# Kernel optimization log

Measured on AMD Instinct MI355X. Metric: run time of the kernel, lower is better.

## Reference

```python
import jax, jax.numpy as jnp
import numpy as np


def _conv3x3(x, w):
    # x: [B,Cin,H,W], w: [Cout,Cin,3,3], stride 1, pad 1
    return jax.lax.conv_general_dilated(x, w, window_strides=(1, 1), padding='SAME',
                                        dimension_numbers=('NCHW', 'OIHW', 'NCHW'))


def _affine(x, s, b):
    # per-channel folded eval-mode BatchNorm (+ absorbed conv bias)
    return x * s[None, :, None, None] + b[None, :, None, None]


def _lif_encode(h, thr, beta, T=4):
    # LIF integrate-and-fire scan: membrane = beta*m + h; STE spike; soft reset.
    def step(m, _):
        m = beta * m + h
        sig = jax.nn.sigmoid(4.0 * (m - thr))
        hard = (m > thr).astype(h.dtype)
        spk = sig + jax.lax.stop_gradient(hard - sig)  # surrogate-gradient STE
        return m - spk * thr, spk
    _, spikes = jax.lax.scan(step, jnp.zeros_like(h), None, length=T)
    return spikes  # [T,B,C_bot,H,W]


def _level(feat, ew, ebs, ebb, thr, braw, dw, dbs, dbb):
    h = _affine(_conv3x3(feat, ew), ebs, ebb)
    spikes = _lif_encode(h, thr, jax.nn.sigmoid(braw))
    avg = spikes.mean(axis=0)  # ber=0.0 -> BSC channel is identity
    return jax.nn.silu(_affine(_conv3x3(avg, dw), dbs, dbb))


def _forward(feat3, enc3_w, enc3_bn_s, enc3_bn_b, enc3_thr, enc3_beta_raw, dec3_w, dec3_bn_s, dec3_bn_b,
             feat4, enc4_w, enc4_bn_s, enc4_bn_b, enc4_thr, enc4_beta_raw, dec4_w, dec4_bn_s, dec4_bn_b,
             feat5, enc5_w, enc5_bn_s, enc5_bn_b, enc5_thr, enc5_beta_raw, dec5_w, dec5_bn_s, dec5_bn_b):
    r3 = _level(feat3, enc3_w, enc3_bn_s, enc3_bn_b, enc3_thr, enc3_beta_raw, dec3_w, dec3_bn_s, dec3_bn_b)
    r4 = _level(feat4, enc4_w, enc4_bn_s, enc4_bn_b, enc4_thr, enc4_beta_raw, dec4_w, dec4_bn_s, dec4_bn_b)
    r5 = _level(feat5, enc5_w, enc5_bn_s, enc5_bn_b, enc5_thr, enc5_beta_raw, dec5_w, dec5_bn_s, dec5_bn_b)
    return (r3, r4, r5)


def setup_inputs() -> dict:
    key = jax.random.key(0)
    C_bot, B = 36, 16
    levels = {3: (64, 160), 4: (128, 80), 5: (256, 40)}
    inp = {}
    k = key
    for lvl, (c, s) in levels.items():
        k, k1, k2, k3 = jax.random.split(k, 4)
        inp[f'feat{lvl}'] = jax.random.normal(k1, (B, c, s, s), jnp.float32)
        inp[f'enc{lvl}_w'] = jax.random.normal(k2, (C_bot, c, 3, 3), jnp.float32) / np.float32(np.sqrt(9 * c))
        inp[f'enc{lvl}_bn_s'] = jnp.ones((C_bot,), jnp.float32)
        inp[f'enc{lvl}_bn_b'] = jnp.zeros((C_bot,), jnp.float32)
        inp[f'enc{lvl}_thr'] = jnp.ones((1, C_bot, 1, 1), jnp.float32)
        inp[f'enc{lvl}_beta_raw'] = jnp.full((1, C_bot, 1, 1), 2.2, jnp.float32)
        inp[f'dec{lvl}_w'] = jax.random.normal(k3, (c, C_bot, 3, 3), jnp.float32) / np.float32(np.sqrt(9 * C_bot))
        inp[f'dec{lvl}_bn_s'] = jnp.ones((c,), jnp.float32)
        inp[f'dec{lvl}_bn_b'] = jnp.zeros((c,), jnp.float32)
    return inp


def reference(feat3, enc3_w, enc3_bn_s, enc3_bn_b, enc3_thr, enc3_beta_raw, dec3_w, dec3_bn_s, dec3_bn_b,
              feat4, enc4_w, enc4_bn_s, enc4_bn_b, enc4_thr, enc4_beta_raw, dec4_w, dec4_bn_s, dec4_bn_b,
              feat5, enc5_w, enc5_bn_s, enc5_bn_b, enc5_thr, enc5_beta_raw, dec5_w, dec5_bn_s, dec5_bn_b):
    return _forward(feat3, enc3_w, enc3_bn_s, enc3_bn_b, enc3_thr, enc3_beta_raw, dec3_w, dec3_bn_s, dec3_bn_b,
                    feat4, enc4_w, enc4_bn_s, enc4_bn_b, enc4_thr, enc4_beta_raw, dec4_w, dec4_bn_s, dec4_bn_b,
                    feat5, enc5_w, enc5_bn_s, enc5_bn_b, enc5_thr, enc5_beta_raw, dec5_w, dec5_bn_s, dec5_bn_b)
```

## Files before the change

### kernel.cpp

```cpp
#include <hip/hip_runtime.h>
#include <hip/hip_bf16.h>

typedef __attribute__((ext_vector_type(8)))  short short8v;
typedef __attribute__((ext_vector_type(16))) float f32x16;
typedef __attribute__((ext_vector_type(4)))  int   int4v;

template<int CIN>
__global__ __launch_bounds__(256) void pack_we(
    const float* __restrict__ w, __hip_bfloat16* __restrict__ whi,
    __hip_bfloat16* __restrict__ wlo, int total)
{
    const int NCHUNK = CIN / 16;
    int idx = blockIdx.x * 256 + threadIdx.x;
    if (idx >= total) return;
    int m  = idx & 31;
    int h  = (idx >> 5) & 1;
    int s  = (idx >> 6) % 9;
    int c  = (idx / 576) % NCHUNK;
    int cg = idx / (576 * NCHUNK);
    int co = cg * 32 + m;
    unsigned short vh[8], vl[8];
    #pragma unroll
    for (int j = 0; j < 8; ++j) {
        int ci = c * 16 + h * 8 + j;
        float x = (co < 36) ? w[(long)co * CIN * 9 + ci * 9 + s] : 0.f;
        __hip_bfloat16 xh = __float2bfloat16(x);
        float rem = x - __bfloat162float(xh);
        __hip_bfloat16 xl = __float2bfloat16(rem);
        vh[j] = *(unsigned short*)&xh;
        vl[j] = *(unsigned short*)&xl;
    }
    *(int4v*)(whi + (long)idx * 8) = *(int4v*)vh;
    *(int4v*)(wlo + (long)idx * 8) = *(int4v*)vl;
}

template<int CIN>
__global__ __launch_bounds__(256) void feat_cl(
    const float* __restrict__ f, __hip_bfloat16* __restrict__ fh,
    __hip_bfloat16* __restrict__ fl, int HW, int npx)
{
    __shared__ float t[CIN][64];
    const int p0 = blockIdx.x * 64;

    for (int i = threadIdx.x; i < CIN * 64; i += 256) {
        int ci = i >> 6, px = i & 63;
        int p = p0 + px;
        float v = 0.f;
        if (p < npx) {
            int b = p / HW, r = p - b * HW;
            v = f[((long)b * CIN + ci) * HW + r];
        }
        t[ci][px] = v;
    }
    __syncthreads();

    for (int i = threadIdx.x; i < 64 * (CIN / 8); i += 256) {
        int px = i & 63, oct = i >> 6;
        int p = p0 + px;
        if (p >= npx) continue;
        unsigned short vh[8], vl[8];
        #pragma unroll
        for (int j = 0; j < 8; ++j) {
            float v = t[oct * 8 + j][px];
            __hip_bfloat16 xh = __float2bfloat16(v);
            float rem = v - __bfloat162float(xh);
            __hip_bfloat16 xl = __float2bfloat16(rem);
            vh[j] = *(unsigned short*)&xh;
            vl[j] = *(unsigned short*)&xl;
        }
        *(int4v*)(fh + (long)p * CIN + oct * 8) = *(int4v*)vh;
        *(int4v*)(fl + (long)p * CIN + oct * 8) = *(int4v*)vl;
    }
}

template<int CIN>
__global__ __launch_bounds__(256) void enc_mfma_cl(
    const __hip_bfloat16* __restrict__ fh,
    const __hip_bfloat16* __restrict__ fl,
    const __hip_bfloat16* __restrict__ whi,
    const __hip_bfloat16* __restrict__ wlo,
    const float* __restrict__ bn_s, const float* __restrict__ bn_b,
    const float* __restrict__ thr, const float* __restrict__ beta_raw,
    __hip_bfloat16* __restrict__ avg,
    int H, int W, int tiles_x)
{
    const int NCHUNK = CIN / 16;
    __shared__ __align__(16) short sbuf[324 * 48];
    short* hi_t = sbuf;
    short* lo_t = sbuf + 324 * 24;

    const int tid = threadIdx.x;
    const int b   = blockIdx.y;
    const int tx0 = (blockIdx.x % tiles_x) * 16;
    const int ty0 = (blockIdx.x / tiles_x) * 16;

    const int lane = tid & 63;
    const int wv   = tid >> 6;
    const int h    = lane >> 5;
    const int n    = lane & 31;
    const int lx   = n & 15;
    const int ly0  = wv * 4 + (n >> 4);

    f32x16 acc[2][2];
    #pragma unroll
    for (int cg = 0; cg < 2; ++cg)
        #pragma unroll
        for (int pf = 0; pf < 2; ++pf)
            #pragma unroll
            for (int k = 0; k < 16; ++k) acc[cg][pf][k] = 0.f;

    const char* aph = (const char*)whi + h * 512 + n * 16;
    const char* apl = (const char*)wlo + h * 512 + n * 16;
    const long  cgstride = (long)NCHUNK * 9216;

    for (int c = 0; c < NCHUNK; ++c) {
        for (int i = tid; i < 648; i += 256) {
            int p   = i >> 1, oct = i & 1;
            int hy = p / 18, hx = p - hy * 18;
            int gy = ty0 + hy - 1, gx = tx0 + hx - 1;
            int4v vh = {0, 0, 0, 0}, vl = {0, 0, 0, 0};
            if (gy >= 0 && gy < H && gx >= 0 && gx < W) {
                long pp = ((long)(b * H + gy) * W + gx) * CIN + c * 16 + oct * 8;
                vh = *(const int4v*)(fh + pp);
                vl = *(const int4v*)(fl + pp);
            }
            *(int4v*)((char*)hi_t + p * 48 + oct * 16) = vh;
            *(int4v*)((char*)lo_t + p * 48 + oct * 16) = vl;
        }
        __syncthreads();

        const char* ahc = aph + (long)c * 9216;
        const char* alc = apl + (long)c * 9216;
        #pragma unroll
        for (int s = 0; s < 9; ++s) {
            const int dy = s / 3, dx = s % 3;
            const int p0 = (ly0 + dy) * 18 + (lx + dx);
            const int p1 = p0 + 36;
            short8v bh0 = *(const short8v*)((const char*)hi_t + p0 * 48 + h * 16);
            short8v bh1 = *(const short8v*)((const char*)hi_t + p1 * 48 + h * 16);
            short8v bl0 = *(const short8v*)((const char*)lo_t + p0 * 48 + h * 16);
            short8v bl1 = *(const short8v*)((const char*)lo_t + p1 * 48 + h * 16);
            #pragma unroll
            for (int cg = 0; cg < 2; ++cg) {
                short8v af = *(const short8v*)(ahc + cg * cgstride + s * 1024);
                short8v al = *(const short8v*)(alc + cg * cgstride + s * 1024);
                acc[cg][0] = __builtin_amdgcn_mfma_f32_32x32x16_bf16(af, bh0, acc[cg][0], 0, 0, 0);
                acc[cg][0] = __builtin_amdgcn_mfma_f32_32x32x16_bf16(af, bl0, acc[cg][0], 0, 0, 0);
                acc[cg][0] = __builtin_amdgcn_mfma_f32_32x32x16_bf16(al, bh0, acc[cg][0], 0, 0, 0);
                acc[cg][1] = __builtin_amdgcn_mfma_f32_32x32x16_bf16(af, bh1, acc[cg][1], 0, 0, 0);
                acc[cg][1] = __builtin_amdgcn_mfma_f32_32x32x16_bf16(af, bl1, acc[cg][1], 0, 0, 0);
                acc[cg][1] = __builtin_amdgcn_mfma_f32_32x32x16_bf16(al, bh1, acc[cg][1], 0, 0, 0);
            }
        }
        __syncthreads();
    }

    for (int i = tid; i < 1280; i += 256)
        *(int4v*)((char*)sbuf + i * 16) = (int4v){0, 0, 0, 0};
    __syncthreads();

    #pragma unroll
    for (int cg = 0; cg < 2; ++cg) {
        #pragma unroll
        for (int r = 0; r < 16; ++r) {
            const int co = (cg << 5) + (r & 3) + ((r >> 2) << 3) + (h << 2);
            if (co < 36) {
                const float sc   = bn_s[co], sb = bn_b[co];
                const float beta = 1.f / (1.f + expf(-beta_raw[co]));
                const float t    = thr[co];
                #pragma unroll
                for (int pf = 0; pf < 2; ++pf) {
                    const int ly = ly0 + pf * 2;
                    float hv = acc[cg][pf][r] * sc + sb;
                    float m = 0.f, c2 = 0.f;
                    #pragma unroll
                    for (int s4 = 0; s4 < 4; ++s4) {
                        m = beta * m + hv;
                        if (m > t) { c2 += 1.f; m -= t; }
                    }
                    __hip_bfloat16 ov = __float2bfloat16(c2 * 0.25f);
                    sbuf[(ly * 16 + lx) * 40 + co] = *(short*)&ov;
                }
            }
        }
    }
    __syncthreads();

    const long tilebase = ((long)(b * H + ty0) * W + tx0) * 40;
    for (int i = tid; i < 1280; i += 256) {
        int px = i / 5, u = i - px * 5;
        int py2 = px >> 4, px2 = px & 15;
        *(int4v*)(avg + tilebase + ((long)py2 * W + px2) * 40 + u * 8) =
            *(const int4v*)(sbuf + px * 40 + u * 8);
    }
}

template<int CIN>
__global__ __launch_bounds__(256) void enc_mfma(
    const float* __restrict__ feat,
    const __hip_bfloat16* __restrict__ whi,
    const __hip_bfloat16* __restrict__ wlo,
    const float* __restrict__ bn_s, const float* __restrict__ bn_b,
    const float* __restrict__ thr, const float* __restrict__ beta_raw,
    __hip_bfloat16* __restrict__ avg,
    int H, int W, int tiles_x)
{
    const int NCHUNK = CIN / 16;
    __shared__ __align__(16) short hi_t[324 * 24];
    __shared__ __align__(16) short lo_t[324 * 24];

    const int tid = threadIdx.x;
    const int b   = blockIdx.y;
    const int tx0 = (blockIdx.x % tiles_x) * 16;
    const int ty0 = (blockIdx.x / tiles_x) * 16;

    const int lane = tid & 63;
    const int wv   = tid >> 6;
    const int h    = lane >> 5;
    const int n    = lane & 31;
    const int lx   = n & 15;
    const int ly0  = wv * 4 + (n >> 4);

    f32x16 acc[2][2];
    #pragma unroll
    for (int cg = 0; cg < 2; ++cg)
        #pragma unroll
        for (int pf = 0; pf < 2; ++pf)
            #pragma unroll
            for (int k = 0; k < 16; ++k) acc[cg][pf][k] = 0.f;

    const float* fb = feat + (long)b * CIN * H * W;
    const char* aph = (const char*)whi + h * 512 + n * 16;
    const char* apl = (const char*)wlo + h * 512 + n * 16;
    const long  cgstride = (long)NCHUNK * 9216;

    for (int c = 0; c < NCHUNK; ++c) {
        for (int i = tid; i < 324 * 16; i += 256) {
            int cil = i / 324;
            int p   = i - cil * 324;
            int hy = p / 18, hx = p - hy * 18;
            int gy = ty0 + hy - 1, gx = tx0 + hx - 1;
            float v = 0.f;
            if (gy >= 0 && gy < H && gx >= 0 && gx < W)
                v = fb[((long)(c * 16 + cil) * H + gy) * W + gx];
            __hip_bfloat16 vh = __float2bfloat16(v);
            float rem = v - __bfloat162float(vh);
            __hip_bfloat16 vl = __float2bfloat16(rem);
            hi_t[p * 24 + cil] = *(short*)&vh;
            lo_t[p * 24 + cil] = *(short*)&vl;
        }
        __syncthreads();

        const char* ahc = aph + (long)c * 9216;
        const char* alc = apl + (long)c * 9216;
        #pragma unroll
        for (int s = 0; s < 9; ++s) {
            const int dy = s / 3, dx = s % 3;
            const int p0 = (ly0 + dy) * 18 + (lx + dx);
            const int p1 = p0 + 36;
            short8v bh0 = *(const short8v*)((const char*)hi_t + p0 * 48 + h * 16);
            short8v bh1 = *(const short8v*)((const char*)hi_t + p1 * 48 + h * 16);
            short8v bl0 = *(const short8v*)((const char*)lo_t + p0 * 48 + h * 16);
            short8v bl1 = *(const short8v*)((const char*)lo_t + p1 * 48 + h * 16);
            #pragma unroll
            for (int cg = 0; cg < 2; ++cg) {
                short8v af = *(const short8v*)(ahc + cg * cgstride + s * 1024);
                short8v al = *(const short8v*)(alc + cg * cgstride + s * 1024);
                acc[cg][0] = __builtin_amdgcn_mfma_f32_32x32x16_bf16(af, bh0, acc[cg][0], 0, 0, 0);
                acc[cg][0] = __builtin_amdgcn_mfma_f32_32x32x16_bf16(af, bl0, acc[cg][0], 0, 0, 0);
                acc[cg][0] = __builtin_amdgcn_mfma_f32_32x32x16_bf16(al, bh0, acc[cg][0], 0, 0, 0);
                acc[cg][1] = __builtin_amdgcn_mfma_f32_32x32x16_bf16(af, bh1, acc[cg][1], 0, 0, 0);
                acc[cg][1] = __builtin_amdgcn_mfma_f32_32x32x16_bf16(af, bl1, acc[cg][1], 0, 0, 0);
                acc[cg][1] = __builtin_amdgcn_mfma_f32_32x32x16_bf16(al, bh1, acc[cg][1], 0, 0, 0);
            }
        }
        __syncthreads();
    }

    #pragma unroll
    for (int cg = 0; cg < 2; ++cg) {
        #pragma unroll
        for (int r = 0; r < 16; ++r) {
            const int co = (cg << 5) + (r & 3) + ((r >> 2) << 3) + (h << 2);
            if (co < 36) {
                const float sc   = bn_s[co], sb = bn_b[co];
                const float beta = 1.f / (1.f + expf(-beta_raw[co]));
                const float t    = thr[co];
                #pragma unroll
                for (int pf = 0; pf < 2; ++pf) {
                    const int gy = ty0 + ly0 + pf * 2, gx = tx0 + lx;
                    float hv = acc[cg][pf][r] * sc + sb;
                    float m = 0.f, c2 = 0.f;
                    #pragma unroll
                    for (int s4 = 0; s4 < 4; ++s4) {
                        m = beta * m + hv;
                        if (m > t) { c2 += 1.f; m -= t; }
                    }
                    if (gy < H && gx < W)
                        avg[((long)(b * H + gy) * W + gx) * 40 + co] =
                            __float2bfloat16(c2 * 0.25f);
                }
            }
        }
    }
}

template<int CIN, int CIPER, int CICHUNK, int COCHUNK, int TDIM, bool PARTIAL, bool CL>
__global__ __launch_bounds__(TDIM* TDIM) void enc_tiled(
    const float* __restrict__ feat,
    const float* __restrict__ w,
    const float* __restrict__ bn_s, const float* __restrict__ bn_b,
    const float* __restrict__ thr, const float* __restrict__ beta_raw,
    __hip_bfloat16* __restrict__ avg,
    float* __restrict__ partial,
    int H, int W, int tiles_x)
{
    const int TPB  = TDIM * TDIM;
    const int HALOD = TDIM + 2;
    const int NCO  = 36 / COCHUNK;
    __shared__ float fs[CICHUNK][HALOD][HALOD];

    const int tile = blockIdx.x;
    const int b    = blockIdx.y;
    const int coc  = blockIdx.z % NCO;
    const int cis  = blockIdx.z / NCO;
    const int co0  = coc * COCHUNK;
    const int tx0  = (tile % tiles_x) * TDIM;
    const int ty0  = (tile / tiles_x) * TDIM;

    const int tx = threadIdx.x % TDIM;
    const int ty = threadIdx.x / TDIM;
    const int ox = tx0 + tx, oy = ty0 + ty;

    float acc[COCHUNK];
    #pragma unroll
    for (int c = 0; c < COCHUNK; ++c) acc[c] = 0.f;

    const float* fb = feat + (long)b * CIN * H * W;
    const int ci_base = cis * CIPER;

    for (int cc = ci_base; cc < ci_base + CIPER; cc += CICHUNK) {
        for (int i = threadIdx.x; i < CICHUNK * HALOD * HALOD; i += TPB) {
            int ci = i / (HALOD * HALOD);
            int r  = i % (HALOD * HALOD);
            int hy = r / HALOD, hx = r % HALOD;
            int gy = ty0 + hy - 1, gx = tx0 + hx - 1;
            float v = 0.f;
            if (gy >= 0 && gy < H && gx >= 0 && gx < W)
                v = fb[((long)(cc + ci) * H + gy) * W + gx];
            fs[ci][hy][hx] = v;
        }
        __syncthreads();

        for (int ci = 0; ci < CICHUNK; ++ci) {
            float f0 = fs[ci][ty    ][tx], f1 = fs[ci][ty    ][tx+1], f2 = fs[ci][ty    ][tx+2];
            float f3 = fs[ci][ty + 1][tx], f4 = fs[ci][ty + 1][tx+1], f5 = fs[ci][ty + 1][tx+2];
            float f6 = fs[ci][ty + 2][tx], f7 = fs[ci][ty + 2][tx+1], f8 = fs[ci][ty + 2][tx+2];
            const float* wq = w + (long)(cc + ci) * 9;
            #pragma unroll
            for (int j = 0; j < COCHUNK; ++j) {
                const float* ww = wq + (long)(co0 + j) * CIN * 9;
                acc[j] += f0 * ww[0] + f1 * ww[1] + f2 * ww[2]
                        + f3 * ww[3] + f4 * ww[4] + f5 * ww[5]
                        + f6 * ww[6] + f7 * ww[7] + f8 * ww[8];
            }
        }
        __syncthreads();
    }

    if (ox < W && oy < H) {
        if (PARTIAL) {
            #pragma unroll
            for (int j = 0; j < COCHUNK; ++j)
                partial[((((long)cis * 16 + b) * 36 + (co0 + j)) * H + oy) * W + ox] = acc[j];
        } else {
            float cnt[COCHUNK];
            #pragma unroll
            for (int j = 0; j < COCHUNK; ++j) {
                int co = co0 + j;
                float hh   = acc[j] * bn_s[co] + bn_b[co];
                float beta = 1.f / (1.f + expf(-beta_raw[co]));
                float t    = thr[co];
                float m = 0.f, c2 = 0.f;
                #pragma unroll
                for (int s = 0; s < 4; ++s) {
                    m = beta * m + hh;
                    if (m > t) { c2 += 1.f; m -= t; }
                }
                cnt[j] = c2 * 0.25f;
            }
            if (CL) {
                unsigned* dp = (unsigned*)(avg + ((long)(b * H + oy) * W + ox) * 40 + co0);
                #pragma unroll
                for (int j2 = 0; j2 < COCHUNK / 2; ++j2) {
                    __hip_bfloat16 h0 = __float2bfloat16(cnt[2 * j2]);
                    __hip_bfloat16 h1 = __float2bfloat16(cnt[2 * j2 + 1]);
                    unsigned u0 = *(unsigned short*)&h0;
                    unsigned u1 = *(unsigned short*)&h1;
                    dp[j2] = u0 | (u1 << 16);
                }
            } else {
                #pragma unroll
                for (int j = 0; j < COCHUNK; ++j)
                    avg[(((long)b * 36 + (co0 + j)) * H + oy) * W + ox] = __float2bfloat16(cnt[j]);
            }
        }
    }
}

template<int SPLITS, bool CL>
__global__ __launch_bounds__(256) void combine_lif(
    const float* __restrict__ partial,
    const float* __restrict__ bn_s, const float* __restrict__ bn_b,
    const float* __restrict__ thr, const float* __restrict__ beta_raw,
    __hip_bfloat16* __restrict__ avg, int H, int W, int total)
{
    int idx = blockIdx.x * 256 + threadIdx.x;
    if (idx >= total) return;
    int HW = H * W;
    int co = (idx / HW) % 36;
    float hh = 0.f;
    #pragma unroll
    for (int s = 0; s < SPLITS; ++s) hh += partial[(long)s * total + idx];
    hh = hh * bn_s[co] + bn_b[co];
    float beta = 1.f / (1.f + expf(-beta_raw[co]));
    float t    = thr[co];
    float m = 0.f, cnt = 0.f;
    #pragma unroll
    for (int s = 0; s < 4; ++s) {
        m = beta * m + hh;
        if (m > t) { cnt += 1.f; m -= t; }
    }
    if (CL) {
        int b = idx / (36 * HW);
        int rem = idx % HW;
        int y = rem / W, x = rem % W;
        avg[((long)(b * H + y) * W + x) * 40 + co] = __float2bfloat16(cnt * 0.25f);
    } else {
        avg[idx] = __float2bfloat16(cnt * 0.25f);
    }
}

__global__ __launch_bounds__(256) void pack_w(
    const float* __restrict__ w, __hip_bfloat16* __restrict__ ap, int total)
{
    int idx = blockIdx.x * 256 + threadIdx.x;
    if (idx >= total) return;
    int m  = idx & 31;
    int h  = (idx >> 5) & 1;
    int s  = (idx >> 6) % 23;
    int cg = idx / (23 * 64);
    int o  = 2 * s + h;
    int co = cg * 32 + m;
    unsigned short v[8];
    #pragma unroll
    for (int j = 0; j < 8; ++j) {
        float x = 0.f;
        if (o < 45) {
            int tap = o / 5, oct = o % 5, ci = oct * 8 + j;
            if (ci < 36) x = w[(long)co * 324 + ci * 9 + tap];
        }
        __hip_bfloat16 hv = __float2bfloat16(x);
        v[j] = *(unsigned short*)&hv;
    }
    *(int4v*)(ap + (long)idx * 8) = *(int4v*)v;
}

template<int COG>
__global__ __launch_bounds__(256) void dec_mfma(
    const __hip_bfloat16* __restrict__ avg_cl,
    const __hip_bfloat16* __restrict__ apack,
    const float* __restrict__ bn_s, const float* __restrict__ bn_b,
    float* __restrict__ out, int Cout, int H, int W, int tiles_x)
{
    __shared__ __hip_bfloat16 tile[12960];

    const int tid    = threadIdx.x;
    const int b      = blockIdx.y;
    const int cgbase = blockIdx.z * COG;
    const int tx0 = (blockIdx.x % tiles_x) * 16;
    const int ty0 = (blockIdx.x / tiles_x) * 16;

    {
        const __hip_bfloat16* ab = avg_cl + (long)b * H * W * 40;
        for (int i = tid; i < 1620; i += 256) {
            int row = i / 90, u = i - row * 90;
            int px = u / 5, un = u - px * 5;
            int gy = ty0 + row - 1, gx = tx0 + px - 1;
            int4v v = {0, 0, 0, 0};
            if (gy >= 0 && gy < H && gx >= 0 && gx < W)
                v = *(const int4v*)(ab + ((long)gy * W + gx) * 40 + un * 8);
            *(int4v*)(tile + (row * 18 + px) * 40 + un * 8) = v;
        }
    }
    __syncthreads();

    const int lane = tid & 63;
    const int wv   = tid >> 6;
    const int h    = lane >> 5;
    const int n    = lane & 31;
    const int lx   = n & 15;
    const int ly0  = wv * 4 + (n >> 4);

    const char* tb  = (const char*)tile;
    const int   bb0 = ((ly0 + 1) * 18 + (lx + 1)) * 80;
    const int   bb1 = bb0 + 2 * 18 * 80;

    const char* ap = (const char*)apack + (long)cgbase * 23552 + h * 512 + n * 16;

    f32x16 acc[COG][2];
    #pragma unroll
    for (int cg = 0; cg < COG; ++cg)
        #pragma unroll
        for (int pf = 0; pf < 2; ++pf)
            #pragma unroll
            for (int k = 0; k < 16; ++k) acc[cg][pf][k] = 0.f;

    #pragma unroll
    for (int s = 0; s < 23; ++s) {
        int o0 = 2 * s;     if (o0 > 44) o0 = 44;
        int o1 = 2 * s + 1; if (o1 > 44) o1 = 44;
        const int C0 = ((o0 / 5) / 3 - 1) * 1440 + ((o0 / 5) % 3 - 1) * 80 + (o0 % 5) * 16;
        const int C1 = ((o1 / 5) / 3 - 1) * 1440 + ((o1 / 5) % 3 - 1) * 80 + (o1 % 5) * 16;
        const int offc = h ? C1 : C0;
        short8v bf0 = *(const short8v*)(tb + (bb0 + offc));
        short8v bf1 = *(const short8v*)(tb + (bb1 + offc));
        #pragma unroll
        for (int cg = 0; cg < COG; ++cg) {
            short8v af = *(const short8v*)(ap + cg * 23552 + s * 1024);
            acc[cg][0] = __builtin_amdgcn_mfma_f32_32x32x16_bf16(af, bf0, acc[cg][0], 0, 0, 0);
            acc[cg][1] = __builtin_amdgcn_mfma_f32_32x32x16_bf16(af, bf1, acc[cg][1], 0, 0, 0);
        }
    }

    #pragma unroll
    for (int cg = 0; cg < COG; ++cg) {
        #pragma unroll
        for (int r = 0; r < 16; ++r) {
            const int co = ((cgbase + cg) << 5) + (r & 3) + ((r >> 2) << 3) + (h << 2);
            const float sc = bn_s[co], bc = bn_b[co];
            #pragma unroll
            for (int pf = 0; pf < 2; ++pf) {
                const int ly = ly0 + pf * 2;
                const int gy = ty0 + ly, gx = tx0 + lx;
                float v = acc[cg][pf][r] * sc + bc;
                v = v / (1.f + __expf(-v));
                if (gy < H && gx < W)
                    out[(((long)b * Cout + co) * H + gy) * W + gx] = v;
            }
        }
    }
}

template<int COCHUNK, int TDIM>
__global__ __launch_bounds__(TDIM* TDIM) void dec_tiled(
    const __hip_bfloat16* __restrict__ avg,
    const float* __restrict__ w,
    const float* __restrict__ bn_s, const float* __restrict__ bn_b,
    float* __restrict__ out,
    int Cout, int H, int W, int tiles_x)
{
    const int CIN = 36;
    const int TPB = TDIM * TDIM;
    const int HALOD = TDIM + 2;
    __shared__ float fs[CIN][HALOD][HALOD];

    const int tile = blockIdx.x;
    const int b    = blockIdx.y;
    const int co0  = blockIdx.z * COCHUNK;
    const int tx0  = (tile % tiles_x) * TDIM;
    const int ty0  = (tile / tiles_x) * TDIM;

    const int tx = threadIdx.x % TDIM;
    const int ty = threadIdx.x / TDIM;
    const int ox = tx0 + tx, oy = ty0 + ty;

    const __hip_bfloat16* ab = avg + (long)b * CIN * H * W;

    for (int i = threadIdx.x; i < CIN * HALOD * HALOD; i += TPB) {
        int ci = i / (HALOD * HALOD);
        int r  = i % (HALOD * HALOD);
        int hy = r / HALOD, hx = r % HALOD;
        int gy = ty0 + hy - 1, gx = tx0 + hx - 1;
        float v = 0.f;
        if (gy >= 0 && gy < H && gx >= 0 && gx < W)
            v = __bfloat162float(ab[((long)ci * H + gy) * W + gx]);
        fs[ci][hy][hx] = v;
    }
    __syncthreads();

    float acc[COCHUNK];
    #pragma unroll
    for (int j = 0; j < COCHUNK; ++j) acc[j] = 0.f;

    for (int ci = 0; ci < CIN; ++ci) {
        float f0 = fs[ci][ty    ][tx], f1 = fs[ci][ty    ][tx+1], f2 = fs[ci][ty    ][tx+2];
        float f3 = fs[ci][ty + 1][tx], f4 = fs[ci][ty + 1][tx+1], f5 = fs[ci][ty + 1][tx+2];
        float f6 = fs[ci][ty + 2][tx], f7 = fs[ci][ty + 2][tx+1], f8 = fs[ci][ty + 2][tx+2];
        #pragma unroll
        for (int j = 0; j < COCHUNK; ++j) {
            const float* ww = w + ((long)(co0 + j) * CIN + ci) * 9;
            acc[j] += f0 * ww[0] + f1 * ww[1] + f2 * ww[2]
                    + f3 * ww[3] + f4 * ww[4] + f5 * ww[5]
                    + f6 * ww[6] + f7 * ww[7] + f8 * ww[8];
        }
    }

    if (ox < W && oy < H) {
        #pragma unroll
        for (int j = 0; j < COCHUNK; ++j) {
            int co = co0 + j;
            float v = acc[j] * bn_s[co] + bn_b[co];
            out[(((long)b * Cout + co) * H + oy) * W + ox] = v / (1.f + expf(-v));
        }
    }
}

extern "C" void kernel_launch(void* const* d_in, const int* in_sizes, int n_in,
                              void* d_out, int out_size, void* d_ws, size_t ws_size,
                              hipStream_t stream)
{
    const int B = 16;
    const int C[3] = {64, 128, 256};
    const int S[3] = {160, 80, 40};

    float* out = (float*)d_out;
    long out_off[3]; long off = 0;
    for (int l = 0; l < 3; ++l) { out_off[l] = off; off += (long)B * C[l] * S[l] * S[l]; }

    const long avgcl_bytes[3] = {32768000L, 8192000L, 2048000L};
    long avgcl_off[3]; long boff = 0;
    for (int l = 0; l < 3; ++l) { avgcl_off[l] = boff; boff += avgcl_bytes[l]; }
    const long avgcl_total = boff;
    const long ap_bytes[3] = {47104L, 94208L, 188416L};
    long ap_off[3];
    for (int l = 0; l < 3; ++l) { ap_off[l] = boff; boff += ap_bytes[l]; }
    const long we_bytes[3] = {73728L, 147456L, 294912L};
    long wehi_off[3], welo_off[3];
    for (int l = 0; l < 3; ++l) { wehi_off[l] = boff; boff += we_bytes[l];
                                  welo_off[l] = boff; boff += we_bytes[l]; }
    const long part5_off = boff;
    const long part5_bytes = 4L * B * 36 * 1600 * 4;
    boff += part5_bytes;
    const size_t need_full = (size_t)boff;
    const size_t need_min  = (size_t)part5_off;
    const long fcl_bytes[2] = {52428800L, 26214400L};
    long fclhi_off[2], fcllo_off[2];
    for (int l = 0; l < 2; ++l) { fclhi_off[l] = boff; boff += fcl_bytes[l];
                                  fcllo_off[l] = boff; boff += fcl_bytes[l]; }
    const size_t need_cl = (size_t)boff;

    char* wsb = (char*)d_ws;

    if (ws_size >= need_min) {
        const bool split5 = ws_size >= need_full;
        const bool use_cl = ws_size >= need_cl;
        hipMemsetAsync(wsb, 0, avgcl_total, stream);

        for (int l = 0; l < 3; ++l) {
            const float* dec_w = (const float*)d_in[9 * l + 6];
            int total = (C[l] / 32) * 23 * 2 * 32;
            pack_w<<<(total + 255) / 256, 256, 0, stream>>>(
                dec_w, (__hip_bfloat16*)(wsb + ap_off[l]), total);
        }
        {
            const float* enc_w3 = (const float*)d_in[1];
            int total = 2 * (64 / 16) * 9 * 2 * 32;
            pack_we<64><<<(total + 255) / 256, 256, 0, stream>>>(
                enc_w3, (__hip_bfloat16*)(wsb + wehi_off[0]),
                (__hip_bfloat16*)(wsb + welo_off[0]), total);
        }
        {
            const float* enc_w4 = (const float*)d_in[10];
            int total = 2 * (128 / 16) * 9 * 2 * 32;
            pack_we<128><<<(total + 255) / 256, 256, 0, stream>>>(
                enc_w4, (__hip_bfloat16*)(wsb + wehi_off[1]),
                (__hip_bfloat16*)(wsb + welo_off[1]), total);
        }
        if (use_cl) {
            {
                int HW = 160 * 160, npx = B * HW;
                feat_cl<64><<<(npx + 63) / 64, 256, 0, stream>>>(
                    (const float*)d_in[0], (__hip_bfloat16*)(wsb + fclhi_off[0]),
                    (__hip_bfloat16*)(wsb + fcllo_off[0]), HW, npx);
            }
            {
                int HW = 80 * 80, npx = B * HW;
                feat_cl<128><<<(npx + 63) / 64, 256, 0, stream>>>(
                    (const float*)d_in[9], (__hip_bfloat16*)(wsb + fclhi_off[1]),
                    (__hip_bfloat16*)(wsb + fcllo_off[1]), HW, npx);
            }
        }

        for (int l = 0; l < 3; ++l) {
            const int base = 9 * l;
            const float* feat     = (const float*)d_in[base + 0];
            const float* enc_w    = (const float*)d_in[base + 1];
            const float* enc_bn_s = (const float*)d_in[base + 2];
            const float* enc_bn_b = (const float*)d_in[base + 3];
            const float* enc_thr  = (const float*)d_in[base + 4];
            const float* enc_beta = (const float*)d_in[base + 5];
            const float* dec_bn_s = (const float*)d_in[base + 7];
            const float* dec_bn_b = (const float*)d_in[base + 8];

            const int Hs = S[l], Wsz = S[l];
            __hip_bfloat16* avg_cl = (__hip_bfloat16*)(wsb + avgcl_off[l]);
            const __hip_bfloat16* ap = (const __hip_bfloat16*)(wsb + ap_off[l]);
            float* r = out + out_off[l];

            if (l == 0) {
                dim3 eg(100, B);
                if (use_cl)
                    enc_mfma_cl<64><<<eg, 256, 0, stream>>>(
                        (const __hip_bfloat16*)(wsb + fclhi_off[0]),
                        (const __hip_bfloat16*)(wsb + fcllo_off[0]),
                        (const __hip_bfloat16*)(wsb + wehi_off[0]),
                        (const __hip_bfloat16*)(wsb + welo_off[0]),
                        enc_bn_s, enc_bn_b, enc_thr, enc_beta, avg_cl, Hs, Wsz, 10);
                else
                    enc_mfma<64><<<eg, 256, 0, stream>>>(
                        feat, (const __hip_bfloat16*)(wsb + wehi_off[0]),
                        (const __hip_bfloat16*)(wsb + welo_off[0]),
                        enc_bn_s, enc_bn_b, enc_thr, enc_beta, avg_cl, Hs, Wsz, 10);
                dim3 dg(100, B, 1);
                dec_mfma<2><<<dg, 256, 0, stream>>>(avg_cl, ap, dec_bn_s, dec_bn_b, r, 64, Hs, Wsz, 10);
            } else if (l == 1) {
                dim3 eg(25, B);
                if (use_cl)
                    enc_mfma_cl<128><<<eg, 256, 0, stream>>>(
                        (const __hip_bfloat16*)(wsb + fclhi_off[1]),
                        (const __hip_bfloat16*)(wsb + fcllo_off[1]),
                        (const __hip_bfloat16*)(wsb + wehi_off[1]),
                        (const __hip_bfloat16*)(wsb + welo_off[1]),
                        enc_bn_s, enc_bn_b, enc_thr, enc_beta, avg_cl, Hs, Wsz, 5);
                else
                    enc_mfma<128><<<eg, 256, 0, stream>>>(
                        feat, (const __hip_bfloat16*)(wsb + wehi_off[1]),
                        (const __hip_bfloat16*)(wsb + welo_off[1]),
                        enc_bn_s, enc_bn_b, enc_thr, enc_beta, avg_cl, Hs, Wsz, 5);
                dim3 dg(25, B, 2);
                dec_mfma<2><<<dg, 256, 0, stream>>>(avg_cl, ap, dec_bn_s, dec_bn_b, r, 128, Hs, Wsz, 5);
            } else {
                if (split5) {
                    float* partial5 = (float*)(wsb + part5_off);
                    dim3 eg(25, B, 12);
                    enc_tiled<256, 64, 16, 12, 8, true, true><<<eg, 64, 0, stream>>>(
                        feat, enc_w, enc_bn_s, enc_bn_b, enc_thr, enc_beta, nullptr, partial5, Hs, Wsz, 5);
                    int total = B * 36 * Hs * Wsz;
                    combine_lif<4, true><<<(total + 255) / 256, 256, 0, stream>>>(
                        partial5, enc_bn_s, enc_bn_b, enc_thr, enc_beta, avg_cl, Hs, Wsz, total);
                } else {
                    dim3 eg(25, B, 3);
                    enc_tiled<256, 256, 16, 12, 8, false, true><<<eg, 64, 0, stream>>>(
                        feat, enc_w, enc_bn_s, enc_bn_b, enc_thr, enc_beta, avg_cl, nullptr, Hs, Wsz, 5);
                }
                dim3 dg(9, B, 4);
                dec_mfma<2><<<dg, 256, 0, stream>>>(avg_cl, ap, dec_bn_s, dec_bn_b, r, 256, Hs, Wsz, 3);
            }
        }
    } else {
        __hip_bfloat16* ws = (__hip_bfloat16*)d_ws;
        long avg_off2[3]; long eoff = 0;
        for (int l = 0; l < 3; ++l) { avg_off2[l] = eoff; eoff += (long)B * 36 * S[l] * S[l]; }
        float* partial5 = (float*)(ws + ((eoff + 7) & ~7L));
        const long part5f = 4L * B * 36 * 40 * 40;
        const size_t old_need = (size_t)((eoff + 7) & ~7L) * 2 + part5f * 4;
        const bool split5 = ws_size >= old_need;

        for (int l = 0; l < 3; ++l) {
            const int base = 9 * l;
            const float* feat     = (const float*)d_in[base + 0];
            const float* enc_w    = (const float*)d_in[base + 1];
            const float* enc_bn_s = (const float*)d_in[base + 2];
            const float* enc_bn_b = (const float*)d_in[base + 3];
            const float* enc_thr  = (const float*)d_in[base + 4];
            const float* enc_beta = (const float*)d_in[base + 5];
            const float* dec_w    = (const float*)d_in[base + 6];
            const float* dec_bn_s = (const float*)d_in[base + 7];
            const float* dec_bn_b = (const float*)d_in[base + 8];

            const int Hs = S[l], Wsz = S[l], Cl = C[l];
            __hip_bfloat16* avg = ws + avg_off2[l];
            float* r = out + out_off[l];

            if (l == 0) {
                dim3 eg(100, B, 3);
                enc_tiled<64, 64, 16, 12, 16, false, false><<<eg, 256, 0, stream>>>(
                    feat, enc_w, enc_bn_s, enc_bn_b, enc_thr, enc_beta, avg, nullptr, Hs, Wsz, 10);
                dim3 dg(100, B, 2);
                dec_tiled<32, 16><<<dg, 256, 0, stream>>>(avg, dec_w, dec_bn_s, dec_bn_b, r, Cl, Hs, Wsz, 10);
            } else if (l == 1) {
                dim3 eg(25, B, 3);
                enc_tiled<128, 128, 16, 12, 16, false, false><<<eg, 256, 0, stream>>>(
                    feat, enc_w, enc_bn_s, enc_bn_b, enc_thr, enc_beta, avg, nullptr, Hs, Wsz, 5);
                dim3 dg(25, B, 4);
                dec_tiled<32, 16><<<dg, 256, 0, stream>>>(avg, dec_w, dec_bn_s, dec_bn_b, r, Cl, Hs, Wsz, 5);
            } else {
                if (split5) {
                    dim3 eg(25, B, 12);
                    enc_tiled<256, 64, 16, 12, 8, true, false><<<eg, 64, 0, stream>>>(
                        feat, enc_w, enc_bn_s, enc_bn_b, enc_thr, enc_beta, nullptr, partial5, Hs, Wsz, 5);
                    int total = B * 36 * Hs * Wsz;
                    combine_lif<4, false><<<(total + 255) / 256, 256, 0, stream>>>(
                        partial5, enc_bn_s, enc_bn_b, enc_thr, enc_beta, avg, Hs, Wsz, total);
                } else {
                    dim3 eg(25, B, 3);
                    enc_tiled<256, 256, 16, 12, 8, false, false><<<eg, 64, 0, stream>>>(
                        feat, enc_w, enc_bn_s, enc_bn_b, enc_thr, enc_beta, avg, nullptr, Hs, Wsz, 5);
                }
                dim3 dg(25, B, 16);
                dec_tiled<16, 8><<<dg, 64, 0, stream>>>(avg, dec_w, dec_bn_s, dec_bn_b, r, Cl, Hs, Wsz, 5);
            }
        }
    }
}
```

Before: 663.3 us.

## Use split-K MFMA encoder on channels-last bf16 features for level 5

Adds a channels-last hi/lo bf16 conversion of the level-5 features, packs the level-5 encoder weights, and runs a new MFMA encoder kernel split into four input-channel groups that write fp32 partial sums. The existing combine_lif kernel then applies BN and the LIF step. This replaces the scalar tiled encoder for the deepest level with matrix-core work and more parallel blocks. The cost is an extra feature transpose pass, more workspace, and partial-sum traffic. The old fp32 enc_mfma fallback is removed and replaced by enc_tiled for levels 3 and 4.

```diff
diff --git a/kernel.cpp b/kernel.cpp
--- a/kernel.cpp
+++ b/kernel.cpp
@@ -34,16 +34,16 @@
     *(int4v*)(wlo + (long)idx * 8) = *(int4v*)vl;
 }
 
-template<int CIN>
+template<int CIN, int PXB>
 __global__ __launch_bounds__(256) void feat_cl(
     const float* __restrict__ f, __hip_bfloat16* __restrict__ fh,
     __hip_bfloat16* __restrict__ fl, int HW, int npx)
 {
-    __shared__ float t[CIN][64];
-    const int p0 = blockIdx.x * 64;
-
-    for (int i = threadIdx.x; i < CIN * 64; i += 256) {
-        int ci = i >> 6, px = i & 63;
+    __shared__ float t[CIN][PXB];
+    const int p0 = blockIdx.x * PXB;
+
+    for (int i = threadIdx.x; i < CIN * PXB; i += 256) {
+        int ci = i / PXB, px = i % PXB;
         int p = p0 + px;
         float v = 0.f;
         if (p < npx) {
@@ -54,8 +54,8 @@
     }
     __syncthreads();
 
-    for (int i = threadIdx.x; i < 64 * (CIN / 8); i += 256) {
-        int px = i & 63, oct = i >> 6;
+    for (int i = threadIdx.x; i < PXB * (CIN / 8); i += 256) {
+        int px = i % PXB, oct = i / PXB;
         int p = p0 + px;
         if (p >= npx) continue;
         unsigned short vh[8], vl[8];
@@ -195,22 +195,24 @@
     }
 }
 
-template<int CIN>
-__global__ __launch_bounds__(256) void enc_mfma(
-    const float* __restrict__ feat,
+template<int CIN, int CIPER>
+__global__ __launch_bounds__(256) void enc_mfma_p(
+    const __hip_bfloat16* __restrict__ fh,
+    const __hip_bfloat16* __restrict__ fl,
     const __hip_bfloat16* __restrict__ whi,
     const __hip_bfloat16* __restrict__ wlo,
-    const float* __restrict__ bn_s, const float* __restrict__ bn_b,
-    const float* __restrict__ thr, const float* __restrict__ beta_raw,
-    __hip_bfloat16* __restrict__ avg,
+    float* __restrict__ partial,
     int H, int W, int tiles_x)
 {
-    const int NCHUNK = CIN / 16;
-    __shared__ __align__(16) short hi_t[324 * 24];
-    __shared__ __align__(16) short lo_t[324 * 24];
+    const int NCH_TOT = CIN / 16;
+    const int NCH_PER = CIPER / 16;
+    __shared__ __align__(16) short sbuf[324 * 48];
+    short* hi_t = sbuf;
+    short* lo_t = sbuf + 324 * 24;
 
     const int tid = threadIdx.x;
     const int b   = blockIdx.y;
+    const int cis = blockIdx.z;
     const int tx0 = (blockIdx.x % tiles_x) * 16;
     const int ty0 = (blockIdx.x / tiles_x) * 16;
 
@@ -229,30 +231,29 @@
             #pragma unroll
             for (int k = 0; k < 16; ++k) acc[cg][pf][k] = 0.f;
 
-    const float* fb = feat + (long)b * CIN * H * W;
     const char* aph = (const char*)whi + h * 512 + n * 16;
     const char* apl = (const char*)wlo + h * 512 + n * 16;
-    const long  cgstride = (long)NCHUNK * 9216;
-
-    for (int c = 0; c < NCHUNK; ++c) {
-        for (int i = tid; i < 324 * 16; i += 256) {
-            int cil = i / 324;
-            int p   = i - cil * 324;
+    const long  cgstride = (long)NCH_TOT * 9216;
+
+    for (int c = 0; c < NCH_PER; ++c) {
+        const int gc = cis * NCH_PER + c;
+        for (int i = tid; i < 648; i += 256) {
+            int p   = i >> 1, oct = i & 1;
             int hy = p / 18, hx = p - hy * 18;
             int gy = ty0 + hy - 1, gx = tx0 + hx - 1;
-            float v = 0.f;
-            if (gy >= 0 && gy < H && gx >= 0 && gx < W)
-                v = fb[((long)(c * 16 + cil) * H + gy) * W + gx];
-            __hip_bfloat16 vh = __float2bfloat16(v);
-            float rem = v - __bfloat162float(vh);
-            __hip_bfloat16 vl = __float2bfloat16(rem);
-            hi_t[p * 24 + cil] = *(short*)&vh;
-            lo_t[p * 24 + cil] = *(short*)&vl;
+            int4v vh = {0, 0, 0, 0}, vl = {0, 0, 0, 0};
+            if (gy >= 0 && gy < H && gx >= 0 && gx < W) {
+                long pp = ((long)(b * H + gy) * W + gx) * CIN + gc * 16 + oct * 8;
+                vh = *(const int4v*)(fh + pp);
+                vl = *(const int4v*)(fl + pp);
+            }
+            *(int4v*)((char*)hi_t + p * 48 + oct * 16) = vh;
+            *(int4v*)((char*)lo_t + p * 48 + oct * 16) = vl;
         }
         __syncthreads();
 
-        const char* ahc = aph + (long)c * 9216;
-        const char* alc = apl + (long)c * 9216;
+        const char* ahc = aph + (long)gc * 9216;
+        const char* alc = apl + (long)gc * 9216;
         #pragma unroll
         for (int s = 0; s < 9; ++s) {
             const int dy = s / 3, dx = s % 3;
@@ -277,28 +278,20 @@
         __syncthreads();
     }
 
+    const int HW = H * W;
+    const long total = (long)16 * 36 * HW;
     #pragma unroll
     for (int cg = 0; cg < 2; ++cg) {
         #pragma unroll
         for (int r = 0; r < 16; ++r) {
             const int co = (cg << 5) + (r & 3) + ((r >> 2) << 3) + (h << 2);
             if (co < 36) {
-                const float sc   = bn_s[co], sb = bn_b[co];
-                const float beta = 1.f / (1.f + expf(-beta_raw[co]));
-                const float t    = thr[co];
                 #pragma unroll
                 for (int pf = 0; pf < 2; ++pf) {
                     const int gy = ty0 + ly0 + pf * 2, gx = tx0 + lx;
-                    float hv = acc[cg][pf][r] * sc + sb;
-                    float m = 0.f, c2 = 0.f;
-                    #pragma unroll
-                    for (int s4 = 0; s4 < 4; ++s4) {
-                        m = beta * m + hv;
-                        if (m > t) { c2 += 1.f; m -= t; }
-                    }
                     if (gy < H && gx < W)
-                        avg[((long)(b * H + gy) * W + gx) * 40 + co] =
-                            __float2bfloat16(c2 * 0.25f);
+                        partial[(long)cis * total + ((long)(b * 36 + co) * HW + gy * W + gx)]
+                            = acc[cg][pf][r];
                 }
             }
         }
@@ -644,17 +637,21 @@
     boff += part5_bytes;
     const size_t need_full = (size_t)boff;
     const size_t need_min  = (size_t)part5_off;
-    const long fcl_bytes[2] = {52428800L, 26214400L};
-    long fclhi_off[2], fcllo_off[2];
+    const long fcl_bytes[3] = {52428800L, 26214400L, 13107200L};
+    long fclhi_off[3], fcllo_off[3];
     for (int l = 0; l < 2; ++l) { fclhi_off[l] = boff; boff += fcl_bytes[l];
                                   fcllo_off[l] = boff; boff += fcl_bytes[l]; }
     const size_t need_cl = (size_t)boff;
+    fclhi_off[2] = boff; boff += fcl_bytes[2];
+    fcllo_off[2] = boff; boff += fcl_bytes[2];
+    const size_t need_cl5 = (size_t)boff;
 
     char* wsb = (char*)d_ws;
 
     if (ws_size >= need_min) {
-        const bool split5 = ws_size >= need_full;
-        const bool use_cl = ws_size >= need_cl;
+        const bool split5  = ws_size >= need_full;
+        const bool use_cl  = ws_size >= need_cl;
+        const bool use_cl5 = ws_size >= need_cl5;
         hipMemsetAsync(wsb, 0, avgcl_total, stream);
 
         for (int l = 0; l < 3; ++l) {
@@ -677,19 +674,32 @@
                 enc_w4, (__hip_bfloat16*)(wsb + wehi_off[1]),
                 (__hip_bfloat16*)(wsb + welo_off[1]), total);
         }
+        if (use_cl5) {
+            const float* enc_w5 = (const float*)d_in[19];
+            int total = 2 * (256 / 16) * 9 * 2 * 32;
+            pack_we<256><<<(total + 255) / 256, 256, 0, stream>>>(
+                enc_w5, (__hip_bfloat16*)(wsb + wehi_off[2]),
+                (__hip_bfloat16*)(wsb + welo_off[2]), total);
+        }
         if (use_cl) {
             {
                 int HW = 160 * 160, npx = B * HW;
-                feat_cl<64><<<(npx + 63) / 64, 256, 0, stream>>>(
+                feat_cl<64, 64><<<(npx + 63) / 64, 256, 0, stream>>>(
                     (const float*)d_in[0], (__hip_bfloat16*)(wsb + fclhi_off[0]),
                     (__hip_bfloat16*)(wsb + fcllo_off[0]), HW, npx);
             }
             {
                 int HW = 80 * 80, npx = B * HW;
-                feat_cl<128><<<(npx + 63) / 64, 256, 0, stream>>>(
+                feat_cl<128, 64><<<(npx + 63) / 64, 256, 0, stream>>>(
                     (const float*)d_in[9], (__hip_bfloat16*)(wsb + fclhi_off[1]),
                     (__hip_bfloat16*)(wsb + fcllo_off[1]), HW, npx);
             }
+        }
+        if (use_cl5) {
+            int HW = 40 * 40, npx = B * HW;
+            feat_cl<256, 32><<<(npx + 31) / 32, 256, 0, stream>>>(
+                (const float*)d_in[18], (__hip_bfloat16*)(wsb + fclhi_off[2]),
+                (__hip_bfloat16*)(wsb + fcllo_off[2]), HW, npx);
         }
 
         for (int l = 0; l < 3; ++l) {
@@ -718,10 +728,8 @@
                         (const __hip_bfloat16*)(wsb + welo_off[0]),
                         enc_bn_s, enc_bn_b, enc_thr, enc_beta, avg_cl, Hs, Wsz, 10);
                 else
-                    enc_mfma<64><<<eg, 256, 0, stream>>>(
-                        feat, (const __hip_bfloat16*)(wsb + wehi_off[0]),
-                        (const __hip_bfloat16*)(wsb + welo_off[0]),
-                        enc_bn_s, enc_bn_b, enc_thr, enc_beta, avg_cl, Hs, Wsz, 10);
+                    enc_tiled<64, 64, 16, 12, 16, false, true><<<dim3(100, B, 3), 256, 0, stream>>>(
+                        feat, enc_w, enc_bn_s, enc_bn_b, enc_thr, enc_beta, avg_cl, nullptr, Hs, Wsz, 10);
                 dim3 dg(100, B, 1);
                 dec_mfma<2><<<dg, 256, 0, stream>>>(avg_cl, ap, dec_bn_s, dec_bn_b, r, 64, Hs, Wsz, 10);
             } else if (l == 1) {
@@ -734,14 +742,24 @@
                         (const __hip_bfloat16*)(wsb + welo_off[1]),
                         enc_bn_s, enc_bn_b, enc_thr, enc_beta, avg_cl, Hs, Wsz, 5);
                 else
-                    enc_mfma<128><<<eg, 256, 0, stream>>>(
-                        feat, (const __hip_bfloat16*)(wsb + wehi_off[1]),
-                        (const __hip_bfloat16*)(wsb + welo_off[1]),
-                        enc_bn_s, enc_bn_b, enc_thr, enc_beta, avg_cl, Hs, Wsz, 5);
+                    enc_tiled<128, 128, 16, 12, 16, false, true><<<dim3(25, B, 3), 256, 0, stream>>>(
+                        feat, enc_w, enc_bn_s, enc_bn_b, enc_thr, enc_beta, avg_cl, nullptr, Hs, Wsz, 5);
                 dim3 dg(25, B, 2);
                 dec_mfma<2><<<dg, 256, 0, stream>>>(avg_cl, ap, dec_bn_s, dec_bn_b, r, 128, Hs, Wsz, 5);
             } else {
-                if (split5) {
+                if (use_cl5) {
+                    float* partial5 = (float*)(wsb + part5_off);
+                    dim3 eg(9, B, 4);
+                    enc_mfma_p<256, 64><<<eg, 256, 0, stream>>>(
+                        (const __hip_bfloat16*)(wsb + fclhi_off[2]),
+                        (const __hip_bfloat16*)(wsb + fcllo_off[2]),
+                        (const __hip_bfloat16*)(wsb + wehi_off[2]),
+                        (const __hip_bfloat16*)(wsb + welo_off[2]),
+                        partial5, Hs, Wsz, 3);
+                    int total = B * 36 * Hs * Wsz;
+                    combine_lif<4, true><<<(total + 255) / 256, 256, 0, stream>>>(
+                        partial5, enc_bn_s, enc_bn_b, enc_thr, enc_beta, avg_cl, Hs, Wsz, total);
+                } else if (split5) {
                     float* partial5 = (float*)(wsb + part5_off);
                     dim3 eg(25, B, 12);
                     enc_tiled<256, 64, 16, 12, 8, true, true><<<eg, 64, 0, stream>>>(
```

Result: faster. 614.7 us (-7.3%).
